# Performance work log

Measured on AMD Instinct MI355X. Metric: run time of the kernel, lower is better.

## Reference

```python
import jax, jax.numpy as jnp
import numpy as np

V, E, H, M = 32000, 512, 1024, 256
B, T, STRIDE = 2, 2048, 4


def setup_inputs() -> dict:
    key = jax.random.key(0)
    ks = jax.random.split(key, 18)
    s = 0.02
    n = jax.random.normal
    return {
        'input_ids': jax.random.randint(ks[0], (B, T), 0, V),
        'emb_weight': n(ks[1], (V, E)) * s,
        'gru_w_ih': n(ks[2], (3 * H, E)) * s,
        'gru_w_hh': n(ks[3], (3 * H, H)) * s,
        'gru_b_ih': n(ks[4], (3 * H,)) * s,
        'gru_b_hh': n(ks[5], (3 * H,)) * s,
        'q_w': n(ks[6], (M, H)) * s, 'q_b': n(ks[7], (M,)) * s,
        'k_w': n(ks[8], (M, H)) * s, 'k_b': n(ks[9], (M,)) * s,
        'hfc_w': n(ks[10], (4 * E, H)) * s, 'hfc_b': n(ks[11], (4 * E,)) * s,
        'hproj_w': n(ks[12], (E, 4 * E)) * s, 'hproj_b': n(ks[13], (E,)) * s,
        'v_w': n(ks[14], (E, E)) * s,
        'gate_w': n(ks[15], (E, H)) * s, 'gate_b': n(ks[16], (E,)) * s,
        'out_bias': jnp.zeros((V,), jnp.float32),
    }


def _gru(x, w_ih, w_hh, b_ih, b_hh):
    # x: [B,T,E] -> states [B,T,H]; single-layer torch GRU, h0 = 0
    h_dim = w_hh.shape[1]
    xg = jnp.einsum('bte,ge->btg', x, w_ih) + b_ih  # [B,T,3H] input gates precomputed

    def step(h, xg_t):
        gi_r, gi_z, gi_n = jnp.split(xg_t, 3, axis=-1)
        gh = h @ w_hh.T + b_hh
        gh_r, gh_z, gh_n = jnp.split(gh, 3, axis=-1)
        r = jax.nn.sigmoid(gi_r + gh_r)
        z = jax.nn.sigmoid(gi_z + gh_z)
        nstate = jnp.tanh(gi_n + r * gh_n)
        h_new = (1.0 - z) * nstate + z * h
        return h_new, h_new

    h0 = jnp.zeros((x.shape[0], h_dim), x.dtype)
    _, hs = jax.lax.scan(step, h0, jnp.swapaxes(xg, 0, 1))
    return jnp.swapaxes(hs, 0, 1)


def reference(input_ids, emb_weight, gru_w_ih, gru_w_hh, gru_b_ih, gru_b_hh,
              q_w, q_b, k_w, k_b, hfc_w, hfc_b, hproj_w, hproj_b,
              v_w, gate_w, gate_b, out_bias):
    emb = emb_weight[input_ids]                              # [B,T,E]
    states = _gru(emb, gru_w_ih, gru_w_hh, gru_b_ih, gru_b_hh)  # [B,T,H]; dropout is identity in eval

    head = jnp.square(jax.nn.relu(states @ hfc_w.T + hfc_b))  # [B,T,4E]
    base = head @ hproj_w.T + hproj_b                          # [B,T,E]

    # stride source pooling
    src_states = states[:, ::STRIDE]                         # [B,S,H]
    src_values = emb[:, ::STRIDE]                            # [B,S,E]
    seq_len = states.shape[1]
    src_pos = jnp.arange(0, seq_len, STRIDE)                 # [S]
    tgt_pos = jnp.arange(seq_len)                            # [T]
    mask = src_pos[None, :] < tgt_pos[:, None]               # [T,S] causal

    qk = states @ q_w.T + q_b                                # [B,T,M]
    mk = src_states @ k_w.T + k_b                            # [B,S,M]
    scores = jnp.einsum('btm,bsm->bts', qk, mk) / jnp.sqrt(jnp.array(M, qk.dtype))
    neg = jnp.finfo(scores.dtype).min
    scores = jnp.where(mask[None], scores, neg)
    att = jax.nn.softmax(scores, axis=-1)
    att = att * mask[None]
    att = att / jnp.maximum(att.sum(axis=-1, keepdims=True), 1e-6)

    retrieved = jnp.einsum('bts,bse->bte', att, src_values @ v_w.T)  # [B,T,E]
    mixed = base + jax.nn.sigmoid(states @ gate_w.T + gate_b) * retrieved
    return mixed @ emb_weight.T + out_bias                   # [B,T,V] tied logits
```

## Files before the change

kernel.cpp:

```cpp
#include <hip/hip_runtime.h>
#include <stdint.h>

typedef unsigned short u16;
typedef unsigned int u32;
typedef unsigned long long u64;
using f32x4 = __attribute__((ext_vector_type(4))) float;
using s16x8 = __attribute__((ext_vector_type(8))) short;
using s16x4 = __attribute__((ext_vector_type(4))) short;

#define DI __device__ __forceinline__

constexpr int kV = 32000, kE = 512, kH = 1024, kM = 256;
constexpr int kB = 2, kT = 2048, kS = 512;
constexpr u64 kWatchdogTicks = 200000000ull;

DI u16 f2bf(float f) {
  u32 u = __float_as_uint(f);
  u32 r = (u + 0x7FFFu + ((u >> 16) & 1u)) >> 16;
  return (u16)r;
}
DI float bf2f(u16 u) { return __uint_as_float(((u32)u) << 16); }

DI void gload_lds16(const void* g, void* l) {
  __builtin_amdgcn_global_load_lds((const __attribute__((address_space(1))) void*)g,
                                   (__attribute__((address_space(3))) void*)l, 16, 0, 0);
}
DI bool wd_expired(u64 t0) {
  return (__builtin_amdgcn_s_memrealtime() - t0) > kWatchdogTicks;
}

__global__ __launch_bounds__(256)
void k_cvt(const float* __restrict__ in, u16* __restrict__ out, int n) {
  const int step = gridDim.x * blockDim.x;
  for (int i = blockIdx.x * blockDim.x + threadIdx.x; i * 4 < n; i += step) {
    f32x4 v = *(const f32x4*)(in + (size_t)i * 4);
    ushort4 o;
    o.x = f2bf(v[0]); o.y = f2bf(v[1]); o.z = f2bf(v[2]); o.w = f2bf(v[3]);
    *(ushort4*)(out + (size_t)i * 4) = o;
  }
}

__global__ __launch_bounds__(128)
void k_embed(const int* __restrict__ ids, const float* __restrict__ W,
             u16* __restrict__ out) {
  const int tok = blockIdx.x;
  const int id = ids[tok];
  f32x4 v = ((const f32x4*)(W + (size_t)id * kE))[threadIdx.x];
  ushort4 o;
  o.x = f2bf(v[0]); o.y = f2bf(v[1]); o.z = f2bf(v[2]); o.w = f2bf(v[3]);
  ((ushort4*)(out + (size_t)tok * kE))[threadIdx.x] = o;
}

__global__ __launch_bounds__(256)
void k_stride_copy(const u16* __restrict__ in, u16* __restrict__ out, int rowlen) {
  const int row = blockIdx.x;
  const int b = row / kS, s = row - b * kS;
  const u16* src = in + ((size_t)b * kT + 4 * s) * rowlen;
  u16* dst = out + (size_t)row * rowlen;
  for (int i = threadIdx.x; i < rowlen / 2; i += blockDim.x)
    reinterpret_cast<u32*>(dst)[i] = reinterpret_cast<const u32*>(src)[i];
}

template<int EPI>
__global__ __launch_bounds__(256)
void k_gemm(const u16* __restrict__ A, const u16* __restrict__ Bm,
            float* __restrict__ Cf, u16* __restrict__ Cb,
            const float* __restrict__ bias,
            int Mdim, int Ndim, int Kdim,
            long long sA, long long sB, long long sC,
            const float* __restrict__ addf, const float* __restrict__ mulf) {
  __shared__ __align__(16) u16 lA[128 * 32];
  __shared__ __align__(16) u16 lB[128 * 32];
  const int tid = threadIdx.x;
  const int bz = blockIdx.z;
  A += (long long)bz * sA;
  Bm += (long long)bz * sB;
  const long long coff = (long long)bz * sC;
  const int m0 = blockIdx.y * 128;
  const int n0 = blockIdx.x * 128;
  const int lane = tid & 63;
  const int wm = ((tid >> 6) >> 1) * 64;
  const int wn = ((tid >> 6) & 1) * 64;
  const int sr = tid >> 2;
  const int sc = (tid & 3) * 8;
  f32x4 acc[4][4] = {};
  for (int kt = 0; kt < Kdim; kt += 32) {
    gload_lds16(A + (long long)(m0 + sr) * Kdim + kt + sc,       &lA[tid * 8]);
    gload_lds16(A + (long long)(m0 + 64 + sr) * Kdim + kt + sc,  &lA[(tid + 256) * 8]);
    gload_lds16(Bm + (long long)(n0 + sr) * Kdim + kt + sc,      &lB[tid * 8]);
    gload_lds16(Bm + (long long)(n0 + 64 + sr) * Kdim + kt + sc, &lB[(tid + 256) * 8]);
    __syncthreads();
    s16x8 af[4], bfv[4];
    const int fro = lane & 15;
    const int fk = (lane >> 4) * 8;
#pragma unroll
    for (int f = 0; f < 4; f++) {
      af[f]  = *reinterpret_cast<const s16x8*>(&lA[(wm + f * 16 + fro) * 32 + fk]);
      bfv[f] = *reinterpret_cast<const s16x8*>(&lB[(wn + f * 16 + fro) * 32 + fk]);
    }
#pragma unroll
    for (int i = 0; i < 4; i++)
#pragma unroll
      for (int j = 0; j < 4; j++)
        acc[i][j] = __builtin_amdgcn_mfma_f32_16x16x32_bf16(af[i], bfv[j], acc[i][j], 0, 0, 0);
    __syncthreads();
  }
  const int crow = (lane >> 4) * 4;
  const int ccol = lane & 15;
#pragma unroll
  for (int i = 0; i < 4; i++) {
#pragma unroll
    for (int j = 0; j < 4; j++) {
      const int gn = n0 + wn + j * 16 + ccol;
      const float bs = bias ? bias[gn] : 0.0f;
#pragma unroll
      for (int r = 0; r < 4; r++) {
        const int gm = m0 + wm + i * 16 + crow + r;
        const long long off = coff + (long long)gm * Ndim + gn;
        float v = acc[i][j][r] + bs;
        if constexpr (EPI == 0) {
          Cf[off] = v;
        } else if constexpr (EPI == 1) {
          Cb[off] = f2bf(v);
        } else if constexpr (EPI == 2) {
          float uu = fmaxf(v, 0.0f);
          Cb[off] = f2bf(uu * uu);
        } else {
          float g = 1.0f / (1.0f + __expf(-v));
          Cb[off] = f2bf(addf[off] + g * mulf[off]);
        }
      }
    }
  }
}

__global__ __launch_bounds__(512, 2)
void k_gru(const float* __restrict__ xg, const u16* __restrict__ whh,
           const float* __restrict__ bhh, u64* __restrict__ hbuf,
           u32* __restrict__ flags, u16* __restrict__ states) {
  extern __shared__ u16 lds_pad[];
  __shared__ __align__(16) float lh[2][1024];
  __shared__ u32 s_ticket, s_dec, s_res, s_bail;
  const int tid = threadIdx.x;
  const u64 wd0 = __builtin_amdgcn_s_memrealtime();
  u32 xcc;
  asm("s_getreg_b32 %0, hwreg(HW_REG_XCC_ID)" : "=s"(xcc));
  xcc &= 7u;
  if (tid == 0) {
    s_bail = 0u;
    u32 tk = atomicAdd(&flags[128 + xcc], 1u);
    if (tk == 31u) {
      u32 fidx = atomicAdd(&flags[136], 1u);
      if (fidx < 2u)
        __hip_atomic_store(&flags[140 + fidx], xcc + 1u, __ATOMIC_RELAXED, __HIP_MEMORY_SCOPE_AGENT);
    }
    s_ticket = tk;
    u32 d = 0;
    if (blockIdx.x == 0) {
      u32 polls = 0;
      for (;;) {
        if (__hip_atomic_load(&flags[136], __ATOMIC_RELAXED, __HIP_MEMORY_SCOPE_AGENT) >= 2u) {
          u32 a = __hip_atomic_load(&flags[140], __ATOMIC_RELAXED, __HIP_MEMORY_SCOPE_AGENT);
          u32 b = __hip_atomic_load(&flags[141], __ATOMIC_RELAXED, __HIP_MEMORY_SCOPE_AGENT);
          if (a && b) { d = 1u | ((a - 1u) << 8) | ((b - 1u) << 16); break; }
        }
        __builtin_amdgcn_s_sleep(1);
        if (++polls > 500000u || wd_expired(wd0)) { d = 2u; break; }
      }
      __hip_atomic_store(&flags[137], d, __ATOMIC_RELAXED, __HIP_MEMORY_SCOPE_AGENT);
    } else {
      u32 polls = 0;
      while (!(d = __hip_atomic_load(&flags[137], __ATOMIC_RELAXED, __HIP_MEMORY_SCOPE_AGENT))) {
        __builtin_amdgcn_s_sleep(1);
        if (++polls > 1000000u || wd_expired(wd0)) { d = 2u; break; }
      }
    }
    s_dec = d;
  }
  __syncthreads();
  const u32 dec = s_dec, ticket = s_ticket;
  int batch = -1;
  u32 slice = 0;
  bool l2m = false;
  if ((dec & 0xFFu) == 1u) {
    const u32 d0 = (dec >> 8) & 0xFFu, d1 = (dec >> 16) & 0xFFu;
    if (xcc == d0 && ticket < 32u) { batch = 0; slice = ticket; l2m = true; }
    else if (xcc == d1 && ticket < 32u) { batch = 1; slice = ticket; l2m = true; }
  } else {
    if (blockIdx.x < 64u) { batch = (int)(blockIdx.x >> 5); slice = blockIdx.x & 31u; }
  }
  if (batch < 0) return;

  if (l2m) {
    u32* hel = &flags[160 + batch * 32];
    u32* vot = &flags[224 + batch * 32];
    if (tid == 0) {
      u32 one = 1u;
      asm volatile("global_store_dword %0, %1, off" :: "v"(&hel[slice]), "v"(one) : "memory");
    }
    bool ok = true;
    if (tid < 32) {
      u32 v = 0, polls = 0;
      const u32* hp = &hel[tid];
      do {
        asm volatile("global_load_dword %0, %1, off nt\n\ts_waitcnt vmcnt(0)"
                     : "=v"(v) : "v"(hp) : "memory");
        if (v) break;
        if (wd_expired(wd0)) break;
      } while (++polls < 200000u);
      ok = (v != 0);
    }
    u64 bad = __ballot(tid < 32 && !ok);
    if (tid == 0)
      __hip_atomic_store(&vot[slice], bad ? 2u : 1u, __ATOMIC_RELAXED, __HIP_MEMORY_SCOPE_AGENT);
    bool vb = false;
    if (tid < 32) {
      u32 v = 0, polls = 0;
      while (!(v = __hip_atomic_load(&vot[tid], __ATOMIC_RELAXED, __HIP_MEMORY_SCOPE_AGENT)))
        if (++polls > 1000000u || wd_expired(wd0)) break;
      vb = (v != 1u);
    }
    u64 anybad = __ballot(tid < 32 && vb);
    if (tid == 0) s_res = (anybad == 0ull) ? 1u : 0u;
    __syncthreads();
    if (s_res == 0u) l2m = false;
  }

  const int j0 = (int)slice * 32;
  const int grp = tid >> 4;
  const int gl = tid & 15;
  const int j = j0 + grp;
  f32x4 wreg[3][16];
#pragma unroll
  for (int g = 0; g < 3; g++) {
    const u16* wrow = whh + (size_t)(g * kH + j) * kH;
#pragma unroll
    for (int i = 0; i < 16; i++) {
      s16x4 w = *(const s16x4*)&wrow[4 * (gl + 16 * i)];
      f32x4 wf;
      wf[0] = bf2f((u16)w[0]); wf[1] = bf2f((u16)w[1]);
      wf[2] = bf2f((u16)w[2]); wf[3] = bf2f((u16)w[3]);
      wreg[g][i] = wf;
    }
  }

  const float bhr = bhh[j], bhz = bhh[kH + j], bhn = bhh[2 * kH + j];
  u32* fl = flags + batch * 64;
  const int fli = tid & 31;
  const float* xgb = xg + (size_t)batch * kT * 3 * kH;
  u16* stb = states + (size_t)batch * kT * kH;
  float hkeep = 0.0f;
  float gi_r = 0.0f, gi_z = 0.0f, gi_n = 0.0f;
  if (gl == 0) { gi_r = xgb[j]; gi_z = xgb[kH + j]; gi_n = xgb[2 * kH + j]; }
  bool bailed = false;

  for (int t = 0; t < kT; t++) {
    u64* hc = hbuf + (size_t)(t & 1) * (kB * kH) + (size_t)batch * kH;
    u64* hn = hbuf + (size_t)((t + 1) & 1) * (kB * kH) + (size_t)batch * kH;
    const u32 want = (u32)t;
    float* lhb = lh[t & 1];
    if (!bailed) {
      u64 v0 = 0, v1 = 0;
      u32 polls = 0;
      if (l2m) {
        const u64* p0 = hc + tid;
        const u64* p1 = hc + tid + 512;
        for (;;) {
          asm volatile(
              "global_load_dwordx2 %0, %2, off nt\n\t"
              "global_load_dwordx2 %1, %3, off nt\n\t"
              "s_waitcnt vmcnt(0)"
              : "=&v"(v0), "=&v"(v1) : "v"(p0), "v"(p1) : "memory");
          if ((u32)(v0 >> 32) >= want && (u32)(v1 >> 32) >= want) break;
          if (++polls > 400000u) { bailed = true; break; }
          if (!(polls & 4095u) && wd_expired(wd0)) { bailed = true; break; }
        }
      } else {
        for (;;) {
          v0 = __hip_atomic_load(hc + tid, __ATOMIC_RELAXED, __HIP_MEMORY_SCOPE_AGENT);
          v1 = __hip_atomic_load(hc + tid + 512, __ATOMIC_RELAXED, __HIP_MEMORY_SCOPE_AGENT);
          if ((u32)(v0 >> 32) >= want && (u32)(v1 >> 32) >= want) break;
          if (++polls > 400000u) { bailed = true; break; }
          if (!(polls & 4095u) && wd_expired(wd0)) { bailed = true; break; }
        }
      }
      lhb[tid] = __uint_as_float((u32)v0);
      lhb[tid + 512] = __uint_as_float((u32)v1);
    }
    if (bailed) s_bail = 1u;
    __syncthreads();
    bailed = (s_bail != 0u);
    if (tid == 0) {
      u32 fv = (u32)(t + 1);
      if (l2m) asm volatile("global_store_dword %0, %1, off" :: "v"(&fl[slice]), "v"(fv) : "memory");
      else __hip_atomic_store(&fl[slice], fv, __ATOMIC_RELAXED, __HIP_MEMORY_SCOPE_AGENT);
    }
    u32 myf = 0;
    if (!bailed) {
      if (l2m) asm volatile("global_load_dword %0, %1, off nt\n\ts_waitcnt vmcnt(0)"
                            : "=v"(myf) : "v"(&fl[fli]) : "memory");
      else myf = __hip_atomic_load(&fl[fli], __ATOMIC_RELAXED, __HIP_MEMORY_SCOPE_AGENT);
    }
    float ar = 0.f, az = 0.f, an = 0.f;
#pragma unroll
    for (int i = 0; i < 16; i++) {
      f32x4 h4 = *(const f32x4*)&lhb[4 * (gl + 16 * i)];
      f32x4 w0 = wreg[0][i], w1 = wreg[1][i], w2 = wreg[2][i];
#pragma unroll
      for (int e = 0; e < 4; e++) {
        ar += w0[e] * h4[e];
        az += w1[e] * h4[e];
        an += w2[e] * h4[e];
      }
    }
#pragma unroll
    for (int m = 8; m >= 1; m >>= 1) {
      ar += __shfl_xor(ar, m, 16);
      az += __shfl_xor(az, m, 16);
      an += __shfl_xor(an, m, 16);
    }
    if (!bailed) {
      u32 polls = 0;
      while (__ballot(myf < want) != 0ull) {
        if (++polls > 400000u) { bailed = true; break; }
        if (!(polls & 4095u) && wd_expired(wd0)) { bailed = true; break; }
        if (l2m) asm volatile("global_load_dword %0, %1, off nt\n\ts_waitcnt vmcnt(0)"
                              : "=v"(myf) : "v"(&fl[fli]) : "memory");
        else myf = __hip_atomic_load(&fl[fli], __ATOMIC_RELAXED, __HIP_MEMORY_SCOPE_AGENT);
      }
    }
    if (gl == 0) {
      float r = 1.0f / (1.0f + __expf(-(gi_r + ar + bhr)));
      float z = 1.0f / (1.0f + __expf(-(gi_z + az + bhz)));
      float ex = __expf(2.0f * (gi_n + r * (an + bhn)));
      float n = (ex - 1.0f) / (ex + 1.0f);
      float hnew = (1.0f - z) * n + z * hkeep;
      hkeep = hnew;
      u64 pk = ((u64)(u32)(t + 1) << 32) | (u64)__float_as_uint(hnew);
      if (l2m) asm volatile("global_store_dwordx2 %0, %1, off" :: "v"(hn + j), "v"(pk) : "memory");
      else __hip_atomic_store(hn + j, pk, __ATOMIC_RELAXED, __HIP_MEMORY_SCOPE_AGENT);
      stb[(size_t)t * kH + j] = f2bf(hnew);
      if (t + 1 < kT) {
        const float* xp = xgb + (size_t)(t + 1) * 3 * kH;
        gi_r = xp[j]; gi_z = xp[kH + j]; gi_n = xp[2 * kH + j];
      }
    }
  }
  (void)lds_pad;
}

__global__ __launch_bounds__(256)
void k_softmax(const float* __restrict__ sc, u16* __restrict__ att) {
  const int row = blockIdx.x * 4 + (threadIdx.x >> 6);
  const int lane = threadIdx.x & 63;
  const int t = row & (kT - 1);
  const int nv = (t + 3) >> 2;
  const float* src = sc + (long long)row * kS;
  u16* dst = att + (long long)row * kS;
  f32x4 v0 = *(const f32x4*)(src + lane * 8);
  f32x4 v1 = *(const f32x4*)(src + lane * 8 + 4);
  float x[8];
  float mx = -3.0e38f;
#pragma unroll
  for (int e = 0; e < 8; e++) {
    float val = ((e < 4) ? v0[e & 3] : v1[e & 3]) * 0.0625f;
    x[e] = val;
    if (lane * 8 + e < nv) mx = fmaxf(mx, val);
  }
#pragma unroll
  for (int m = 32; m >= 1; m >>= 1) mx = fmaxf(mx, __shfl_xor(mx, m, 64));
  float p[8];
  float sum = 0.0f;
#pragma unroll
  for (int e = 0; e < 8; e++) {
    p[e] = (lane * 8 + e < nv) ? __expf(x[e] - mx) : 0.0f;
    sum += p[e];
  }
#pragma unroll
  for (int m = 32; m >= 1; m >>= 1) sum += __shfl_xor(sum, m, 64);
  const float inv = (nv == 0) ? 0.0f : (1.0f / sum);
  ushort4 o0, o1;
  o0.x = f2bf(p[0] * inv); o0.y = f2bf(p[1] * inv);
  o0.z = f2bf(p[2] * inv); o0.w = f2bf(p[3] * inv);
  o1.x = f2bf(p[4] * inv); o1.y = f2bf(p[5] * inv);
  o1.z = f2bf(p[6] * inv); o1.w = f2bf(p[7] * inv);
  *(ushort4*)(dst + lane * 8) = o0;
  *(ushort4*)(dst + lane * 8 + 4) = o1;
}

static void gemm(int epi, const u16* A, const u16* Bm, float* Cf, u16* Cb,
                 const float* bias, int M, int N, int K, int batch,
                 long long sA, long long sB, long long sC,
                 const float* addf, const float* mulf, hipStream_t st) {
  dim3 g((unsigned)(N / 128), (unsigned)(M / 128), (unsigned)batch), b(256);
  switch (epi) {
    case 0: k_gemm<0><<<g, b, 0, st>>>(A, Bm, Cf, Cb, bias, M, N, K, sA, sB, sC, addf, mulf); break;
    case 1: k_gemm<1><<<g, b, 0, st>>>(A, Bm, Cf, Cb, bias, M, N, K, sA, sB, sC, addf, mulf); break;
    case 2: k_gemm<2><<<g, b, 0, st>>>(A, Bm, Cf, Cb, bias, M, N, K, sA, sB, sC, addf, mulf); break;
    default: k_gemm<3><<<g, b, 0, st>>>(A, Bm, Cf, Cb, bias, M, N, K, sA, sB, sC, addf, mulf); break;
  }
}

extern "C" void kernel_launch(void* const* d_in, const int* in_sizes, int n_in,
                              void* d_out, int out_size, void* d_ws, size_t ws_size,
                              hipStream_t stream) {
  (void)in_sizes; (void)n_in; (void)out_size;
  const int* ids      = (const int*)d_in[0];
  const float* embW   = (const float*)d_in[1];
  const float* w_ih   = (const float*)d_in[2];
  const float* w_hh   = (const float*)d_in[3];
  const float* b_ih   = (const float*)d_in[4];
  const float* b_hh   = (const float*)d_in[5];
  const float* q_w    = (const float*)d_in[6];
  const float* q_b    = (const float*)d_in[7];
  const float* k_w    = (const float*)d_in[8];
  const float* k_b    = (const float*)d_in[9];
  const float* hfc_w  = (const float*)d_in[10];
  const float* hfc_b  = (const float*)d_in[11];
  const float* hproj_w  = (const float*)d_in[12];
  const float* hproj_b  = (const float*)d_in[13];
  const float* v_w    = (const float*)d_in[14];
  const float* gate_w = (const float*)d_in[15];
  const float* gate_b = (const float*)d_in[16];
  const float* out_b  = (const float*)d_in[17];
  float* out = (float*)d_out;

  char* ws = (char*)d_ws;
  size_t off = 0;
  auto alloc = [&](size_t bytes) -> void* {
    void* p = ws + off;
    off += (bytes + 255) & ~(size_t)255;
    return p;
  };
  u16* embw_bf   = (u16*)alloc((size_t)kV * kE * 2);
  u16* states_bf = (u16*)alloc((size_t)kB * kT * kH * 2);
  u16* emb_bf    = (u16*)alloc((size_t)kB * kT * kE * 2);
  u16* qw_bf     = (u16*)alloc((size_t)kM * kH * 2);
  u16* kw_bf     = (u16*)alloc((size_t)kM * kH * 2);
  u16* hfcw_bf   = (u16*)alloc((size_t)4 * kE * kH * 2);
  u16* hprojw_bf = (u16*)alloc((size_t)kE * 4 * kE * 2);
  u16* vw_bf     = (u16*)alloc((size_t)kE * kE * 2);
  u16* gatew_bf  = (u16*)alloc((size_t)kE * kH * 2);
  u64* hbuf      = (u64*)alloc((size_t)2 * kB * kH * 8);
  u32* flags     = (u32*)alloc(2048);
  const size_t s0 = off;
  u16* wih_bf    = (u16*)alloc((size_t)3 * kH * kE * 2);
  u16* whh_bf    = (u16*)alloc((size_t)3 * kH * kH * 2);
  float* xg      = (float*)alloc((size_t)kB * kT * 3 * kH * 4);
  const size_t endG = off;
  off = s0;
  u16* head_bf   = (u16*)alloc((size_t)kB * kT * 4 * kE * 2);
  float* basef   = (float*)alloc((size_t)kB * kT * kE * 4);
  u16* qk_bf     = (u16*)alloc((size_t)kB * kT * kM * 2);
  u16* srcs_bf   = (u16*)alloc((size_t)kB * kS * kH * 2);
  u16* srcv_bf   = (u16*)alloc((size_t)kB * kS * kE * 2);
  u16* mk_bf     = (u16*)alloc((size_t)kB * kS * kM * 2);
  float* scoresf = (float*)alloc((size_t)kB * kT * kS * 4);
  u16* att_bf    = (u16*)alloc((size_t)kB * kT * kS * 2);
  u16* svt_bf    = (u16*)alloc((size_t)kB * kE * kS * 2);
  float* retrf   = (float*)alloc((size_t)kB * kT * kE * 4);
  u16* mixed_bf  = (u16*)alloc((size_t)kB * kT * kE * 2);
  const size_t endA = off;
  const size_t need = (endG > endA ? endG : endA);
  if (ws_size < need) return;

  dim3 b256(256);
  k_cvt<<<1024, b256, 0, stream>>>(w_ih, wih_bf, 3 * kH * kE);
  k_cvt<<<1024, b256, 0, stream>>>(w_hh, whh_bf, 3 * kH * kH);
  k_cvt<<<1024, b256, 0, stream>>>(q_w, qw_bf, kM * kH);
  k_cvt<<<1024, b256, 0, stream>>>(k_w, kw_bf, kM * kH);
  k_cvt<<<1024, b256, 0, stream>>>(hfc_w, hfcw_bf, 4 * kE * kH);
  k_cvt<<<1024, b256, 0, stream>>>(hproj_w, hprojw_bf, kE * 4 * kE);
  k_cvt<<<1024, b256, 0, stream>>>(v_w, vw_bf, kE * kE);
  k_cvt<<<1024, b256, 0, stream>>>(gate_w, gatew_bf, kE * kH);
  k_cvt<<<2048, b256, 0, stream>>>(embW, embw_bf, kV * kE);
  k_embed<<<kB * kT, 128, 0, stream>>>(ids, embW, emb_bf);

  gemm(0, emb_bf, wih_bf, xg, nullptr, b_ih, kB * kT, 3 * kH, kE,
       1, 0, 0, 0, nullptr, nullptr, stream);

  hipMemsetAsync(hbuf, 0, (size_t)2 * kB * kH * 8 + 2048, stream);
  k_gru<<<256, dim3(512), 96 * 1024, stream>>>(xg, whh_bf, b_hh, hbuf, flags, states_bf);

  gemm(2, states_bf, hfcw_bf, nullptr, head_bf, hfc_b, kB * kT, 4 * kE, kH,
       1, 0, 0, 0, nullptr, nullptr, stream);
  gemm(0, head_bf, hprojw_bf, basef, nullptr, hproj_b, kB * kT, kE, 4 * kE,
       1, 0, 0, 0, nullptr, nullptr, stream);
  gemm(1, states_bf, qw_bf, nullptr, qk_bf, q_b, kB * kT, kM, kH,
       1, 0, 0, 0, nullptr, nullptr, stream);
  k_stride_copy<<<kB * kS, b256, 0, stream>>>(states_bf, srcs_bf, kH);
  k_stride_copy<<<kB * kS, b256, 0, stream>>>(emb_bf, srcv_bf, kE);
  gemm(1, srcs_bf, kw_bf, nullptr, mk_bf, k_b, kB * kS, kM, kH,
       1, 0, 0, 0, nullptr, nullptr, stream);
  gemm(0, qk_bf, mk_bf, scoresf, nullptr, nullptr, kT, kS, kM, kB,
       (long long)kT * kM, (long long)kS * kM, (long long)kT * kS,
       nullptr, nullptr, stream);
  k_softmax<<<(kB * kT) / 4, b256, 0, stream>>>(scoresf, att_bf);
  gemm(1, vw_bf, srcv_bf, nullptr, svt_bf, nullptr, kE, kS, kE, kB,
       0, (long long)kS * kE, (long long)kE * kS, nullptr, nullptr, stream);
  gemm(0, att_bf, svt_bf, retrf, nullptr, nullptr, kT, kE, kS, kB,
       (long long)kT * kS, (long long)kE * kS, (long long)kT * kE,
       nullptr, nullptr, stream);
  gemm(3, states_bf, gatew_bf, nullptr, mixed_bf, gate_b, kB * kT, kE, kH,
       1, 0, 0, 0, basef, retrf, stream);
  gemm(0, mixed_bf, embw_bf, out, nullptr, out_b, kB * kT, kV, kE,
       1, 0, 0, 0, nullptr, nullptr, stream);
}
```

Before: 4.234 ms.

## Compute GRU recurrent matvec with bf16 MFMA using hi/lo split of hidden state

Replaces the per-thread fp32 FMA dot products for the recurrent W_hh·h product with MFMA 16x16x32 bf16 instructions. Six waves each hold a 16-row slice of one gate's weights in registers, and the hidden state is split into bf16 hi and lo parts so precision stays close to fp32. Partial sums are staged through LDS and a dedicated wave finishes the gate nonlinearity. This adds an extra __syncthreads per step and concentrates the flag polling and elementwise update on one wave, changing the per-step latency profile of the serial recurrence.

Measured after the change: 4.911 ms. 16.0% more time.

```diff
diff --git a/kernel.cpp b/kernel.cpp
--- a/kernel.cpp
+++ b/kernel.cpp
@@ -134,12 +134,35 @@
   }
 }
 
+#define DECLF8(P) s16x8 P##0, P##1, P##2, P##3, P##4, P##5, P##6, P##7
+#define LOADF8(P, BASEOFF) \
+  P##0 = *(const s16x8*)(wbase + (BASEOFF + 0) * 32); \
+  P##1 = *(const s16x8*)(wbase + (BASEOFF + 1) * 32); \
+  P##2 = *(const s16x8*)(wbase + (BASEOFF + 2) * 32); \
+  P##3 = *(const s16x8*)(wbase + (BASEOFF + 3) * 32); \
+  P##4 = *(const s16x8*)(wbase + (BASEOFF + 4) * 32); \
+  P##5 = *(const s16x8*)(wbase + (BASEOFF + 5) * 32); \
+  P##6 = *(const s16x8*)(wbase + (BASEOFF + 6) * 32); \
+  P##7 = *(const s16x8*)(wbase + (BASEOFF + 7) * 32)
+#define PIN8(P) asm volatile("" : "+v"(P##0), "+v"(P##1), "+v"(P##2), "+v"(P##3), \
+                                  "+v"(P##4), "+v"(P##5), "+v"(P##6), "+v"(P##7))
+#define DOTK(KC, F) { \
+    const s16x8 bh = *(const s16x8*)&hbf_hi[(KC) * 32 + qg8]; \
+    const s16x8 bl = *(const s16x8*)&hbf_lo[(KC) * 32 + qg8]; \
+    acc0 = __builtin_amdgcn_mfma_f32_16x16x32_bf16(F, bh, acc0, 0, 0, 0); \
+    acc1 = __builtin_amdgcn_mfma_f32_16x16x32_bf16(F, bl, acc1, 0, 0, 0); }
+#define DOT8(B, P) \
+  DOTK(B + 0, P##0) DOTK(B + 1, P##1) DOTK(B + 2, P##2) DOTK(B + 3, P##3) \
+  DOTK(B + 4, P##4) DOTK(B + 5, P##5) DOTK(B + 6, P##6) DOTK(B + 7, P##7)
+
 __global__ __launch_bounds__(512, 2)
 void k_gru(const float* __restrict__ xg, const u16* __restrict__ whh,
            const float* __restrict__ bhh, u64* __restrict__ hbuf,
            u32* __restrict__ flags, u16* __restrict__ states) {
   extern __shared__ u16 lds_pad[];
-  __shared__ __align__(16) float lh[2][1024];
+  __shared__ __align__(16) u16 hbf_hi[1024];
+  __shared__ __align__(16) u16 hbf_lo[1024];
+  __shared__ __align__(16) float sumbuf[96];
   __shared__ u32 s_ticket, s_dec, s_res, s_bail;
   const int tid = threadIdx.x;
   const u64 wd0 = __builtin_amdgcn_s_memrealtime();
@@ -227,38 +250,41 @@
   }
 
   const int j0 = (int)slice * 32;
-  const int grp = tid >> 4;
-  const int gl = tid & 15;
-  const int j = j0 + grp;
-  f32x4 wreg[3][16];
-#pragma unroll
-  for (int g = 0; g < 3; g++) {
-    const u16* wrow = whh + (size_t)(g * kH + j) * kH;
-#pragma unroll
-    for (int i = 0; i < 16; i++) {
-      s16x4 w = *(const s16x4*)&wrow[4 * (gl + 16 * i)];
-      f32x4 wf;
-      wf[0] = bf2f((u16)w[0]); wf[1] = bf2f((u16)w[1]);
-      wf[2] = bf2f((u16)w[2]); wf[3] = bf2f((u16)w[3]);
-      wreg[g][i] = wf;
-    }
-  }
-
-  const float bhr = bhh[j], bhz = bhh[kH + j], bhn = bhh[2 * kH + j];
+  const int wv = tid >> 6;
+  const int lane = tid & 63;
+  const int m16 = lane & 15;
+  const int qg = lane >> 4;
+  const int qg8 = qg * 8;
+
+  DECLF8(fa); DECLF8(fb); DECLF8(fc); DECLF8(fd);
+  int sumbase = 0;
+  if (wv < 6) {
+    const int gate = wv >> 1;
+    const int grow = gate * kH + j0 + (wv & 1) * 16 + m16;
+    const u16* wbase = whh + (size_t)grow * kH + qg8;
+    LOADF8(fa, 0); LOADF8(fb, 8); LOADF8(fc, 16); LOADF8(fd, 24);
+    PIN8(fa); PIN8(fb); PIN8(fc); PIN8(fd);
+    sumbase = gate * 32 + (wv & 1) * 16;
+  }
+
+  const int j = j0 + (lane & 31);
+  float bhr = 0.f, bhz = 0.f, bhn = 0.f;
+  float gi_r = 0.f, gi_z = 0.f, gi_n = 0.f;
+  float hkeep = 0.0f;
   u32* fl = flags + batch * 64;
-  const int fli = tid & 31;
+  const int fli = lane & 31;
   const float* xgb = xg + (size_t)batch * kT * 3 * kH;
   u16* stb = states + (size_t)batch * kT * kH;
-  float hkeep = 0.0f;
-  float gi_r = 0.0f, gi_z = 0.0f, gi_n = 0.0f;
-  if (gl == 0) { gi_r = xgb[j]; gi_z = xgb[kH + j]; gi_n = xgb[2 * kH + j]; }
+  if (wv == 6 && lane < 32) {
+    bhr = bhh[j]; bhz = bhh[kH + j]; bhn = bhh[2 * kH + j];
+    gi_r = xgb[j]; gi_z = xgb[kH + j]; gi_n = xgb[2 * kH + j];
+  }
   bool bailed = false;
 
   for (int t = 0; t < kT; t++) {
     u64* hc = hbuf + (size_t)(t & 1) * (kB * kH) + (size_t)batch * kH;
     u64* hn = hbuf + (size_t)((t + 1) & 1) * (kB * kH) + (size_t)batch * kH;
     const u32 want = (u32)t;
-    float* lhb = lh[t & 1];
     if (!bailed) {
       u64 v0 = 0, v1 = 0;
       u32 polls = 0;
@@ -284,8 +310,13 @@
           if (!(polls & 4095u) && wd_expired(wd0)) { bailed = true; break; }
         }
       }
-      lhb[tid] = __uint_as_float((u32)v0);
-      lhb[tid + 512] = __uint_as_float((u32)v1);
+      const float h0 = __uint_as_float((u32)v0);
+      const float h1 = __uint_as_float((u32)v1);
+      const u16 hi0 = f2bf(h0), hi1 = f2bf(h1);
+      hbf_hi[tid] = hi0;
+      hbf_hi[tid + 512] = hi1;
+      hbf_lo[tid] = f2bf(h0 - bf2f(hi0));
+      hbf_lo[tid + 512] = f2bf(h1 - bf2f(hi1));
     }
     if (bailed) s_bail = 1u;
     __syncthreads();
@@ -295,31 +326,16 @@
       if (l2m) asm volatile("global_store_dword %0, %1, off" :: "v"(&fl[slice]), "v"(fv) : "memory");
       else __hip_atomic_store(&fl[slice], fv, __ATOMIC_RELAXED, __HIP_MEMORY_SCOPE_AGENT);
     }
-    u32 myf = 0;
-    if (!bailed) {
+    if (wv < 6) {
+      f32x4 acc0 = {}, acc1 = {};
+      DOT8(0, fa) DOT8(8, fb) DOT8(16, fc) DOT8(24, fd)
+      f32x4 s = acc0 + acc1;
+      if (m16 == 0) *(f32x4*)&sumbuf[sumbase + qg * 4] = s;
+    } else if (wv == 6 && !bailed) {
+      u32 myf = 0;
       if (l2m) asm volatile("global_load_dword %0, %1, off nt\n\ts_waitcnt vmcnt(0)"
                             : "=v"(myf) : "v"(&fl[fli]) : "memory");
       else myf = __hip_atomic_load(&fl[fli], __ATOMIC_RELAXED, __HIP_MEMORY_SCOPE_AGENT);
-    }
-    float ar = 0.f, az = 0.f, an = 0.f;
-#pragma unroll
-    for (int i = 0; i < 16; i++) {
-      f32x4 h4 = *(const f32x4*)&lhb[4 * (gl + 16 * i)];
-      f32x4 w0 = wreg[0][i], w1 = wreg[1][i], w2 = wreg[2][i];
-#pragma unroll
-      for (int e = 0; e < 4; e++) {
-        ar += w0[e] * h4[e];
-        az += w1[e] * h4[e];
-        an += w2[e] * h4[e];
-      }
-    }
-#pragma unroll
-    for (int m = 8; m >= 1; m >>= 1) {
-      ar += __shfl_xor(ar, m, 16);
-      az += __shfl_xor(az, m, 16);
-      an += __shfl_xor(an, m, 16);
-    }
-    if (!bailed) {
       u32 polls = 0;
       while (__ballot(myf < want) != 0ull) {
         if (++polls > 400000u) { bailed = true; break; }
@@ -329,7 +345,12 @@
         else myf = __hip_atomic_load(&fl[fli], __ATOMIC_RELAXED, __HIP_MEMORY_SCOPE_AGENT);
       }
     }
-    if (gl == 0) {
+    __syncthreads();
+    if (wv == 6 && lane < 32) {
+      const int jj = lane;
+      const float ar = sumbuf[jj];
+      const float az = sumbuf[32 + jj];
+      const float an = sumbuf[64 + jj];
       float r = 1.0f / (1.0f + __expf(-(gi_r + ar + bhr)));
       float z = 1.0f / (1.0f + __expf(-(gi_z + az + bhz)));
       float ex = __expf(2.0f * (gi_n + r * (an + bhn)));
```

## Compute GRU recurrent matvec with MFMA using AGPR-parked bf16 weights

Applied to the files above, without the earlier changes.

The per-step hidden-state matvec in the persistent GRU kernel moves from scalar FP32 FMAs over register-held weights to v_mfma_f32_16x16x32_bf16. The bf16 weight rows are parked in accumulation registers (a0-a127) via inline asm. The hidden state is split into bf16 hi/lo parts so that a spare MFMA row recovers near-fp32 precision. Each wave now produces 4 outputs handled by lane 0, and the 96KB dynamic LDS padding is dropped, which may change occupancy. The aim is to shorten the serial per-step latency, at the cost of a fragile, hand-managed register layout and some accuracy risk.

Measured after the change: 6.830 ms. 1.61x slower.

```diff
diff --git a/kernel.cpp b/kernel.cpp
--- a/kernel.cpp
+++ b/kernel.cpp
@@ -7,6 +7,7 @@
 using f32x4 = __attribute__((ext_vector_type(4))) float;
 using s16x8 = __attribute__((ext_vector_type(8))) short;
 using s16x4 = __attribute__((ext_vector_type(4))) short;
+using u32x4v = __attribute__((ext_vector_type(4))) u32;
 
 #define DI __device__ __forceinline__
 
@@ -134,12 +135,34 @@
   }
 }
 
+#define A_CLOB \
+  "a0","a1","a2","a3","a4","a5","a6","a7","a8","a9","a10","a11","a12","a13","a14","a15", \
+  "a16","a17","a18","a19","a20","a21","a22","a23","a24","a25","a26","a27","a28","a29","a30","a31", \
+  "a32","a33","a34","a35","a36","a37","a38","a39","a40","a41","a42","a43","a44","a45","a46","a47", \
+  "a48","a49","a50","a51","a52","a53","a54","a55","a56","a57","a58","a59","a60","a61","a62","a63", \
+  "a64","a65","a66","a67","a68","a69","a70","a71","a72","a73","a74","a75","a76","a77","a78","a79", \
+  "a80","a81","a82","a83","a84","a85","a86","a87","a88","a89","a90","a91","a92","a93","a94","a95", \
+  "a96","a97","a98","a99","a100","a101","a102","a103","a104","a105","a106","a107","a108","a109","a110","a111", \
+  "a112","a113","a114","a115","a116","a117","a118","a119","a120","a121","a122","a123","a124","a125","a126","a127"
+
+#define AWR(N, V) asm volatile("v_accvgpr_write_b32 a" #N ", %0" :: "v"(V) : "a" #N)
+#define PARK(K, N0, N1, N2, N3) do { \
+    s16x8 f_ = *(const s16x8*)(wbase + (K) * 32); \
+    u32x4v u_ = __builtin_bit_cast(u32x4v, f_); \
+    AWR(N0, u_[0]); AWR(N1, u_[1]); AWR(N2, u_[2]); AWR(N3, u_[3]); } while (0)
+#define MFMA_AG(LO, HI, ACC, B) \
+  asm volatile("v_mfma_f32_16x16x32_bf16 %0, a[" #LO ":" #HI "], %1, %0" \
+               : "+v"(ACC) : "v"(B) : A_CLOB)
+#define STEPK(KC, LO, HI, ACC) do { \
+    const s16x8 b_ = *(const s16x8*)&hbp[(KC) * 32 + qg8]; \
+    MFMA_AG(LO, HI, ACC, b_); } while (0)
+
 __global__ __launch_bounds__(512, 2)
 void k_gru(const float* __restrict__ xg, const u16* __restrict__ whh,
            const float* __restrict__ bhh, u64* __restrict__ hbuf,
            u32* __restrict__ flags, u16* __restrict__ states) {
-  extern __shared__ u16 lds_pad[];
-  __shared__ __align__(16) float lh[2][1024];
+  __shared__ __align__(16) u16 hb_hi[2][1024];
+  __shared__ __align__(16) u16 hb_lo[2][1024];
   __shared__ u32 s_ticket, s_dec, s_res, s_bail;
   const int tid = threadIdx.x;
   const u64 wd0 = __builtin_amdgcn_s_memrealtime();
@@ -227,38 +250,50 @@
   }
 
   const int j0 = (int)slice * 32;
-  const int grp = tid >> 4;
-  const int gl = tid & 15;
-  const int j = j0 + grp;
-  f32x4 wreg[3][16];
-#pragma unroll
-  for (int g = 0; g < 3; g++) {
-    const u16* wrow = whh + (size_t)(g * kH + j) * kH;
-#pragma unroll
-    for (int i = 0; i < 16; i++) {
-      s16x4 w = *(const s16x4*)&wrow[4 * (gl + 16 * i)];
-      f32x4 wf;
-      wf[0] = bf2f((u16)w[0]); wf[1] = bf2f((u16)w[1]);
-      wf[2] = bf2f((u16)w[2]); wf[3] = bf2f((u16)w[3]);
-      wreg[g][i] = wf;
-    }
-  }
-
-  const float bhr = bhh[j], bhz = bhh[kH + j], bhn = bhh[2 * kH + j];
+  const int wv = tid >> 6;
+  const int lane = tid & 63;
+  const int m16 = lane & 15;
+  const int qg8 = (lane >> 4) * 8;
+  const int jbase = j0 + wv * 4;
+
+  {
+    const int grow = (m16 < 12) ? ((m16 >> 2) * kH + jbase + (m16 & 3)) : jbase;
+    const u16* wbase = whh + (size_t)grow * kH + qg8;
+    PARK(0, 0, 1, 2, 3);     PARK(1, 4, 5, 6, 7);     PARK(2, 8, 9, 10, 11);
+    PARK(3, 12, 13, 14, 15); PARK(4, 16, 17, 18, 19); PARK(5, 20, 21, 22, 23);
+    PARK(6, 24, 25, 26, 27); PARK(7, 28, 29, 30, 31); PARK(8, 32, 33, 34, 35);
+    PARK(9, 36, 37, 38, 39); PARK(10, 40, 41, 42, 43); PARK(11, 44, 45, 46, 47);
+    PARK(12, 48, 49, 50, 51); PARK(13, 52, 53, 54, 55); PARK(14, 56, 57, 58, 59);
+    PARK(15, 60, 61, 62, 63); PARK(16, 64, 65, 66, 67); PARK(17, 68, 69, 70, 71);
+    PARK(18, 72, 73, 74, 75); PARK(19, 76, 77, 78, 79); PARK(20, 80, 81, 82, 83);
+    PARK(21, 84, 85, 86, 87); PARK(22, 88, 89, 90, 91); PARK(23, 92, 93, 94, 95);
+    PARK(24, 96, 97, 98, 99); PARK(25, 100, 101, 102, 103); PARK(26, 104, 105, 106, 107);
+    PARK(27, 108, 109, 110, 111); PARK(28, 112, 113, 114, 115); PARK(29, 116, 117, 118, 119);
+    PARK(30, 120, 121, 122, 123); PARK(31, 124, 125, 126, 127);
+  }
+
+  f32x4 bhr4 = {}, bhz4 = {}, bhn4 = {};
+  f32x4 gir4 = {}, giz4 = {}, gin4 = {};
+  f32x4 hk = {};
   u32* fl = flags + batch * 64;
-  const int fli = tid & 31;
+  const int fli = lane & 31;
   const float* xgb = xg + (size_t)batch * kT * 3 * kH;
   u16* stb = states + (size_t)batch * kT * kH;
-  float hkeep = 0.0f;
-  float gi_r = 0.0f, gi_z = 0.0f, gi_n = 0.0f;
-  if (gl == 0) { gi_r = xgb[j]; gi_z = xgb[kH + j]; gi_n = xgb[2 * kH + j]; }
+  if (lane == 0) {
+    bhr4 = *(const f32x4*)&bhh[jbase];
+    bhz4 = *(const f32x4*)&bhh[kH + jbase];
+    bhn4 = *(const f32x4*)&bhh[2 * kH + jbase];
+    gir4 = *(const f32x4*)&xgb[jbase];
+    giz4 = *(const f32x4*)&xgb[kH + jbase];
+    gin4 = *(const f32x4*)&xgb[2 * kH + jbase];
+  }
   bool bailed = false;
 
   for (int t = 0; t < kT; t++) {
     u64* hc = hbuf + (size_t)(t & 1) * (kB * kH) + (size_t)batch * kH;
     u64* hn = hbuf + (size_t)((t + 1) & 1) * (kB * kH) + (size_t)batch * kH;
     const u32 want = (u32)t;
-    float* lhb = lh[t & 1];
+    const int par = t & 1;
     if (!bailed) {
       u64 v0 = 0, v1 = 0;
       u32 polls = 0;
@@ -284,8 +319,13 @@
           if (!(polls & 4095u) && wd_expired(wd0)) { bailed = true; break; }
         }
       }
-      lhb[tid] = __uint_as_float((u32)v0);
-      lhb[tid + 512] = __uint_as_float((u32)v1);
+      const float h0 = __uint_as_float((u32)v0);
+      const float h1 = __uint_as_float((u32)v1);
+      const u16 hi0 = f2bf(h0), hi1 = f2bf(h1);
+      hb_hi[par][tid] = hi0;
+      hb_hi[par][tid + 512] = hi1;
+      hb_lo[par][tid] = f2bf(h0 - bf2f(hi0));
+      hb_lo[par][tid + 512] = f2bf(h1 - bf2f(hi1));
     }
     if (bailed) s_bail = 1u;
     __syncthreads();
@@ -301,23 +341,23 @@
                             : "=v"(myf) : "v"(&fl[fli]) : "memory");
       else myf = __hip_atomic_load(&fl[fli], __ATOMIC_RELAXED, __HIP_MEMORY_SCOPE_AGENT);
     }
-    float ar = 0.f, az = 0.f, an = 0.f;
-#pragma unroll
-    for (int i = 0; i < 16; i++) {
-      f32x4 h4 = *(const f32x4*)&lhb[4 * (gl + 16 * i)];
-      f32x4 w0 = wreg[0][i], w1 = wreg[1][i], w2 = wreg[2][i];
-#pragma unroll
-      for (int e = 0; e < 4; e++) {
-        ar += w0[e] * h4[e];
-        az += w1[e] * h4[e];
-        an += w2[e] * h4[e];
-      }
-    }
-#pragma unroll
-    for (int m = 8; m >= 1; m >>= 1) {
-      ar += __shfl_xor(ar, m, 16);
-      az += __shfl_xor(az, m, 16);
-      an += __shfl_xor(an, m, 16);
+    const u16* hbp = (m16 == 1) ? &hb_lo[par][0] : &hb_hi[par][0];
+    f32x4 acc0 = {}, acc1 = {}, acc2 = {}, acc3 = {};
+    STEPK(0, 0, 3, acc0);    STEPK(8, 32, 35, acc1);   STEPK(16, 64, 67, acc2);   STEPK(24, 96, 99, acc3);
+    STEPK(1, 4, 7, acc0);    STEPK(9, 36, 39, acc1);   STEPK(17, 68, 71, acc2);   STEPK(25, 100, 103, acc3);
+    STEPK(2, 8, 11, acc0);   STEPK(10, 40, 43, acc1);  STEPK(18, 72, 75, acc2);   STEPK(26, 104, 107, acc3);
+    STEPK(3, 12, 15, acc0);  STEPK(11, 44, 47, acc1);  STEPK(19, 76, 79, acc2);   STEPK(27, 108, 111, acc3);
+    STEPK(4, 16, 19, acc0);  STEPK(12, 48, 51, acc1);  STEPK(20, 80, 83, acc2);   STEPK(28, 112, 115, acc3);
+    STEPK(5, 20, 23, acc0);  STEPK(13, 52, 55, acc1);  STEPK(21, 84, 87, acc2);   STEPK(29, 116, 119, acc3);
+    STEPK(6, 24, 27, acc0);  STEPK(14, 56, 59, acc1);  STEPK(22, 88, 91, acc2);   STEPK(30, 120, 123, acc3);
+    STEPK(7, 28, 31, acc0);  STEPK(15, 60, 63, acc1);  STEPK(23, 92, 95, acc2);   STEPK(31, 124, 127, acc3);
+    f32x4 s = (acc0 + acc1) + (acc2 + acc3);
+    float arr[4], azz[4], ann[4];
+#pragma unroll
+    for (int e = 0; e < 4; e++) {
+      arr[e] = __shfl(s[e], 0) + __shfl(s[e], 1);
+      azz[e] = __shfl(s[e], 16) + __shfl(s[e], 17);
+      ann[e] = __shfl(s[e], 32) + __shfl(s[e], 33);
     }
     if (!bailed) {
       u32 polls = 0;
@@ -329,24 +369,30 @@
         else myf = __hip_atomic_load(&fl[fli], __ATOMIC_RELAXED, __HIP_MEMORY_SCOPE_AGENT);
       }
     }
-    if (gl == 0) {
-      float r = 1.0f / (1.0f + __expf(-(gi_r + ar + bhr)));
-      float z = 1.0f / (1.0f + __expf(-(gi_z + az + bhz)));
-      float ex = __expf(2.0f * (gi_n + r * (an + bhn)));
-      float n = (ex - 1.0f) / (ex + 1.0f);
-      float hnew = (1.0f - z) * n + z * hkeep;
-      hkeep = hnew;
-      u64 pk = ((u64)(u32)(t + 1) << 32) | (u64)__float_as_uint(hnew);
-      if (l2m) asm volatile("global_store_dwordx2 %0, %1, off" :: "v"(hn + j), "v"(pk) : "memory");
-      else __hip_atomic_store(hn + j, pk, __ATOMIC_RELAXED, __HIP_MEMORY_SCOPE_AGENT);
-      stb[(size_t)t * kH + j] = f2bf(hnew);
+    if (lane == 0) {
+      u64 spack = 0;
+#pragma unroll
+      for (int o = 0; o < 4; o++) {
+        float r = 1.0f / (1.0f + __expf(-(gir4[o] + arr[o] + bhr4[o])));
+        float z = 1.0f / (1.0f + __expf(-(giz4[o] + azz[o] + bhz4[o])));
+        float ex = __expf(2.0f * (gin4[o] + r * (ann[o] + bhn4[o])));
+        float n = (ex - 1.0f) / (ex + 1.0f);
+        float hnew = (1.0f - z) * n + z * hk[o];
+        hk[o] = hnew;
+        u64 pk = ((u64)(u32)(t + 1) << 32) | (u64)__float_as_uint(hnew);
+        if (l2m) asm volatile("global_store_dwordx2 %0, %1, off" :: "v"(hn + jbase + o), "v"(pk) : "memory");
+        else __hip_atomic_store(hn + jbase + o, pk, __ATOMIC_RELAXED, __HIP_MEMORY_SCOPE_AGENT);
+        spack |= ((u64)f2bf(hnew)) << (16 * o);
+      }
+      *(u64*)&stb[(size_t)t * kH + jbase] = spack;
       if (t + 1 < kT) {
         const float* xp = xgb + (size_t)(t + 1) * 3 * kH;
-        gi_r = xp[j]; gi_z = xp[kH + j]; gi_n = xp[2 * kH + j];
-      }
-    }
-  }
-  (void)lds_pad;
+        gir4 = *(const f32x4*)&xp[jbase];
+        giz4 = *(const f32x4*)&xp[kH + jbase];
+        gin4 = *(const f32x4*)&xp[2 * kH + jbase];
+      }
+    }
+  }
 }
 
 __global__ __launch_bounds__(256)
@@ -480,7 +526,7 @@
        1, 0, 0, 0, nullptr, nullptr, stream);
 
   hipMemsetAsync(hbuf, 0, (size_t)2 * kB * kH * 8 + 2048, stream);
-  k_gru<<<256, dim3(512), 96 * 1024, stream>>>(xg, whh_bf, b_hh, hbuf, flags, states_bf);
+  k_gru<<<256, dim3(512), 0, stream>>>(xg, whh_bf, b_hh, hbuf, flags, states_bf);
 
   gemm(2, states_bf, hfcw_bf, nullptr, head_bf, hfc_b, kB * kT, 4 * kE, kH,
        1, 0, 0, 0, nullptr, nullptr, stream);
```

## Stage GRU recurrent weights as fp16 in LDS, keep n-gate in registers

Applied to the files above, without the earlier changes.

The GRU recurrent kernel previously held all three gate weight slices as fp32 registers (192 floats per thread) converted from bf16. It now converts W_hh to fp16, stages the r and z gate rows in 128KB of static LDS through direct global-to-LDS loads, and keeps only the n gate in packed fp16 registers. The hidden state broadcast is also stored as fp16 in LDS. This cuts register pressure and halves the size of the per-step h reads, but it adds LDS reads of the weights on every timestep, lowers occupancy to one block per CU, and reduces the precision of h to fp16.

Result: slower. 4.899 ms (+15.7%).

```diff
diff --git a/kernel.cpp b/kernel.cpp
--- a/kernel.cpp
+++ b/kernel.cpp
@@ -6,7 +6,7 @@
 typedef unsigned long long u64;
 using f32x4 = __attribute__((ext_vector_type(4))) float;
 using s16x8 = __attribute__((ext_vector_type(8))) short;
-using s16x4 = __attribute__((ext_vector_type(4))) short;
+using h16x8 = __attribute__((ext_vector_type(8))) _Float16;
 
 #define DI __device__ __forceinline__
 
@@ -20,6 +20,7 @@
   return (u16)r;
 }
 DI float bf2f(u16 u) { return __uint_as_float(((u32)u) << 16); }
+DI u16 f2h(float f) { _Float16 h = (_Float16)f; return __builtin_bit_cast(u16, h); }
 
 DI void gload_lds16(const void* g, void* l) {
   __builtin_amdgcn_global_load_lds((const __attribute__((address_space(1))) void*)g,
@@ -36,6 +37,17 @@
     f32x4 v = *(const f32x4*)(in + (size_t)i * 4);
     ushort4 o;
     o.x = f2bf(v[0]); o.y = f2bf(v[1]); o.z = f2bf(v[2]); o.w = f2bf(v[3]);
+    *(ushort4*)(out + (size_t)i * 4) = o;
+  }
+}
+
+__global__ __launch_bounds__(256)
+void k_cvt16(const float* __restrict__ in, u16* __restrict__ out, int n) {
+  const int step = gridDim.x * blockDim.x;
+  for (int i = blockIdx.x * blockDim.x + threadIdx.x; i * 4 < n; i += step) {
+    f32x4 v = *(const f32x4*)(in + (size_t)i * 4);
+    ushort4 o;
+    o.x = f2h(v[0]); o.y = f2h(v[1]); o.z = f2h(v[2]); o.w = f2h(v[3]);
     *(ushort4*)(out + (size_t)i * 4) = o;
   }
 }
@@ -134,12 +146,12 @@
   }
 }
 
-__global__ __launch_bounds__(512, 2)
-void k_gru(const float* __restrict__ xg, const u16* __restrict__ whh,
+__global__ __launch_bounds__(512, 1)
+void k_gru(const float* __restrict__ xg, const u16* __restrict__ whh16,
            const float* __restrict__ bhh, u64* __restrict__ hbuf,
            u32* __restrict__ flags, u16* __restrict__ states) {
-  extern __shared__ u16 lds_pad[];
-  __shared__ __align__(16) float lh[2][1024];
+  __shared__ __align__(16) u16 lw[64 * 1024];
+  __shared__ __align__(16) u16 lh16[2][1024];
   __shared__ u32 s_ticket, s_dec, s_res, s_bail;
   const int tid = threadIdx.x;
   const u64 wd0 = __builtin_amdgcn_s_memrealtime();
@@ -230,19 +242,21 @@
   const int grp = tid >> 4;
   const int gl = tid & 15;
   const int j = j0 + grp;
-  f32x4 wreg[3][16];
-#pragma unroll
-  for (int g = 0; g < 3; g++) {
-    const u16* wrow = whh + (size_t)(g * kH + j) * kH;
-#pragma unroll
-    for (int i = 0; i < 16; i++) {
-      s16x4 w = *(const s16x4*)&wrow[4 * (gl + 16 * i)];
-      f32x4 wf;
-      wf[0] = bf2f((u16)w[0]); wf[1] = bf2f((u16)w[1]);
-      wf[2] = bf2f((u16)w[2]); wf[3] = bf2f((u16)w[3]);
-      wreg[g][i] = wf;
-    }
-  }
+#pragma unroll
+  for (int r = 0; r < 16; r++) {
+    int fi = tid + 512 * r;
+    int rl = fi >> 7;
+    int ce = (fi & 127) * 8;
+    int gate = rl >> 5, jl = rl & 31;
+    gload_lds16(whh16 + ((size_t)gate * kH + j0 + jl) * kH + ce, &lw[fi * 8]);
+  }
+  h16x8 wn8[8];
+  {
+    const _Float16* wnrow = (const _Float16*)(whh16 + (size_t)(2 * kH + j) * kH);
+#pragma unroll
+    for (int i = 0; i < 8; i++) wn8[i] = *(const h16x8*)&wnrow[8 * (gl + 16 * i)];
+  }
+  __syncthreads();
 
   const float bhr = bhh[j], bhz = bhh[kH + j], bhn = bhh[2 * kH + j];
   u32* fl = flags + batch * 64;
@@ -253,12 +267,14 @@
   float gi_r = 0.0f, gi_z = 0.0f, gi_n = 0.0f;
   if (gl == 0) { gi_r = xgb[j]; gi_z = xgb[kH + j]; gi_n = xgb[2 * kH + j]; }
   bool bailed = false;
+  const _Float16* lwr = (const _Float16*)&lw[(size_t)grp * 1024];
+  const _Float16* lwz = (const _Float16*)&lw[(size_t)(32 + grp) * 1024];
 
   for (int t = 0; t < kT; t++) {
     u64* hc = hbuf + (size_t)(t & 1) * (kB * kH) + (size_t)batch * kH;
     u64* hn = hbuf + (size_t)((t + 1) & 1) * (kB * kH) + (size_t)batch * kH;
     const u32 want = (u32)t;
-    float* lhb = lh[t & 1];
+    const int par = t & 1;
     if (!bailed) {
       u64 v0 = 0, v1 = 0;
       u32 polls = 0;
@@ -284,8 +300,8 @@
           if (!(polls & 4095u) && wd_expired(wd0)) { bailed = true; break; }
         }
       }
-      lhb[tid] = __uint_as_float((u32)v0);
-      lhb[tid + 512] = __uint_as_float((u32)v1);
+      lh16[par][tid] = f2h(__uint_as_float((u32)v0));
+      lh16[par][tid + 512] = f2h(__uint_as_float((u32)v1));
     }
     if (bailed) s_bail = 1u;
     __syncthreads();
@@ -301,16 +317,21 @@
                             : "=v"(myf) : "v"(&fl[fli]) : "memory");
       else myf = __hip_atomic_load(&fl[fli], __ATOMIC_RELAXED, __HIP_MEMORY_SCOPE_AGENT);
     }
+    const _Float16* lhh = (const _Float16*)&lh16[par][0];
     float ar = 0.f, az = 0.f, an = 0.f;
 #pragma unroll
-    for (int i = 0; i < 16; i++) {
-      f32x4 h4 = *(const f32x4*)&lhb[4 * (gl + 16 * i)];
-      f32x4 w0 = wreg[0][i], w1 = wreg[1][i], w2 = wreg[2][i];
-#pragma unroll
-      for (int e = 0; e < 4; e++) {
-        ar += w0[e] * h4[e];
-        az += w1[e] * h4[e];
-        an += w2[e] * h4[e];
+    for (int i = 0; i < 8; i++) {
+      const int k = 8 * (gl + 16 * i);
+      h16x8 hv = *(const h16x8*)&lhh[k];
+      h16x8 wr = *(const h16x8*)&lwr[k];
+      h16x8 wz = *(const h16x8*)&lwz[k];
+      h16x8 wn = wn8[i];
+#pragma unroll
+      for (int e = 0; e < 8; e++) {
+        const float hf = (float)hv[e];
+        ar += (float)wr[e] * hf;
+        az += (float)wz[e] * hf;
+        an += (float)wn[e] * hf;
       }
     }
 #pragma unroll
@@ -346,7 +367,6 @@
       }
     }
   }
-  (void)lds_pad;
 }
 
 __global__ __launch_bounds__(256)
@@ -445,7 +465,7 @@
   u32* flags     = (u32*)alloc(2048);
   const size_t s0 = off;
   u16* wih_bf    = (u16*)alloc((size_t)3 * kH * kE * 2);
-  u16* whh_bf    = (u16*)alloc((size_t)3 * kH * kH * 2);
+  u16* whh_h16   = (u16*)alloc((size_t)3 * kH * kH * 2);
   float* xg      = (float*)alloc((size_t)kB * kT * 3 * kH * 4);
   const size_t endG = off;
   off = s0;
@@ -466,7 +486,7 @@
 
   dim3 b256(256);
   k_cvt<<<1024, b256, 0, stream>>>(w_ih, wih_bf, 3 * kH * kE);
-  k_cvt<<<1024, b256, 0, stream>>>(w_hh, whh_bf, 3 * kH * kH);
+  k_cvt16<<<1024, b256, 0, stream>>>(w_hh, whh_h16, 3 * kH * kH);
   k_cvt<<<1024, b256, 0, stream>>>(q_w, qw_bf, kM * kH);
   k_cvt<<<1024, b256, 0, stream>>>(k_w, kw_bf, kM * kH);
   k_cvt<<<1024, b256, 0, stream>>>(hfc_w, hfcw_bf, 4 * kE * kH);
@@ -480,7 +500,7 @@
        1, 0, 0, 0, nullptr, nullptr, stream);
 
   hipMemsetAsync(hbuf, 0, (size_t)2 * kB * kH * 8 + 2048, stream);
-  k_gru<<<256, dim3(512), 96 * 1024, stream>>>(xg, whh_bf, b_hh, hbuf, flags, states_bf);
+  k_gru<<<256, dim3(512), 0, stream>>>(xg, whh_h16, b_hh, hbuf, flags, states_bf);
 
   gemm(2, states_bf, hfcw_bf, nullptr, head_bf, hfc_b, kB * kT, 4 * kE, kH,
        1, 0, 0, 0, nullptr, nullptr, stream);
```
